# Kernel tuning notes

Hardware: AMD Instinct MI355X
Metric: run time of the kernel (lower is better)

Reference implementation:

```python
import jax, jax.numpy as jnp
import numpy as np

VOXEL_SCALE = 20.0   # cfg.SPARSE3D.VOXEL_SCALE (metric -> voxel pixels)
POOLER_SCALE = 0.25  # cfg.MODEL.ROI_BOX_HEAD.POOLER_SCALES_SPATIAL[0]
RES = 7              # pooler resolution per axis
EPS = 1e-5           # BatchNorm eps


def _roi_align_3d(feat, boxes_px, batch_idx, res):
    """3D ROIAlign, sampling_ratio=1 (one trilinear sample per bin).
    feat: [B, X, Y, Z, C] channels-last; boxes_px: [N,6] = (x1,y1,z1,x2,y2,z2)
    in feature-map coordinates. Returns [N, C, res, res, res]."""
    B, X, Y, Z, C = feat.shape
    N = boxes_px.shape[0]
    start, end = boxes_px[:, :3], boxes_px[:, 3:]
    size = jnp.maximum(end - start, 1.0)            # [N,3] legacy min roi size
    binsz = size / res
    off = jnp.arange(res, dtype=boxes_px.dtype) + 0.5
    px = start[:, 0:1] + off[None, :] * binsz[:, 0:1]   # [N,res]
    py = start[:, 1:2] + off[None, :] * binsz[:, 1:2]
    pz = start[:, 2:3] + off[None, :] * binsz[:, 2:3]
    P = res * res * res
    PX = jnp.broadcast_to(px[:, :, None, None], (N, res, res, res)).reshape(N, P)
    PY = jnp.broadcast_to(py[:, None, :, None], (N, res, res, res)).reshape(N, P)
    PZ = jnp.broadcast_to(pz[:, None, None, :], (N, res, res, res)).reshape(N, P)

    def corners(p, dim):
        p0 = jnp.floor(p)
        frac = p - p0
        i0 = jnp.clip(p0.astype(jnp.int32), 0, dim - 1)
        i1 = jnp.clip(p0.astype(jnp.int32) + 1, 0, dim - 1)
        return i0, i1, frac

    x0, x1, lx = corners(PX, X)
    y0, y1, ly = corners(PY, Y)
    z0, z1, lz = corners(PZ, Z)
    feat_flat = feat.reshape(B * X * Y * Z, C)
    base = batch_idx.astype(jnp.int32)[:, None]          # [N,1]
    acc = jnp.zeros((N, P, C), feat.dtype)
    for dx in (0, 1):  # 8 trilinear corners; fixed small loop
        xi, wx = (x0, 1.0 - lx) if dx == 0 else (x1, lx)
        for dy in (0, 1):
            yi, wy = (y0, 1.0 - ly) if dy == 0 else (y1, ly)
            for dz in (0, 1):
                zi, wz = (z0, 1.0 - lz) if dz == 0 else (z1, lz)
                lin = ((base * X + xi) * Y + yi) * Z + zi  # [N,P]
                acc = acc + (wx * wy * wz)[:, :, None] * feat_flat[lin]
    pooled = acc.reshape(N, res, res, res, C)  # 1 sample per bin -> no avg
    return pooled.transpose(0, 4, 1, 2, 3)     # [N, C, rx, ry, rz]


def setup_inputs():
    key = jax.random.key(0)
    ks = jax.random.split(key, 8)
    B, C, X, Y, Z = 2, 128, 80, 80, 20
    N, rep = 1024, 128 * RES              # rep = OUT_CHANNELS * pooler_z = 896
    in_size = C * RES * RES * RES         # 43904
    features = jax.random.normal(ks[0], (B, X, Y, Z, C), jnp.float32)
    ext = jnp.array([16.0, 16.0, 4.0], jnp.float32)  # metric extent = dim/(voxel_scale*pooler_scale)
    ctr = jax.random.uniform(ks[1], (N, 3), jnp.float32) * ext
    half = 0.25 + jax.random.uniform(ks[2], (N, 3), jnp.float32) * 1.75
    boxes = jnp.concatenate([ctr - half, ctr + half], axis=1)  # metric units
    batch_idx = jax.random.randint(ks[3], (N,), 0, B, jnp.int32)
    conv_w = jax.random.normal(ks[4], (rep, C, RES), jnp.float32) * 0.02
    conv_b = jnp.zeros((rep,), jnp.float32)
    gamma = jnp.ones((rep,), jnp.float32)
    beta = jnp.zeros((rep,), jnp.float32)
    fc6_w = jax.random.normal(ks[5], (in_size, rep), jnp.float32) * np.float32(1.0 / np.sqrt(in_size))
    fc6_b = jnp.zeros((rep,), jnp.float32)
    fc7_w = jax.random.normal(ks[6], (rep, rep), jnp.float32) * np.float32(1.0 / np.sqrt(rep))
    fc7_b = jnp.zeros((rep,), jnp.float32)
    return dict(features=features, boxes=boxes, conv_w=conv_w, conv_b=conv_b,
                gamma=gamma, beta=beta, fc6_w=fc6_w, fc6_b=fc6_b,
                fc7_w=fc7_w, fc7_b=fc7_b, batch_idx=batch_idx)


def reference(features, boxes, conv_w, conv_b, gamma, beta,
              fc6_w, fc6_b, fc7_w, fc7_b, batch_idx):
    # convert_metric_to_pixel (x voxel_scale) fused with pooler spatial scale
    boxes_px = boxes * (VOXEL_SCALE * POOLER_SCALE)
    pooled = _roi_align_3d(features, boxes_px, batch_idx, RES)  # [N,C,7,7,7]
    # conv3d kernel [1,1,Z]: contract channels and z -> [N, rep, 7, 7]
    y = jnp.einsum('ncxyz,rcz->nrxy', pooled, conv_w) + conv_b[None, :, None, None]
    # BatchNorm3d, training-mode batch statistics per channel
    mu = y.mean(axis=(0, 2, 3), keepdims=True)
    var = ((y - mu) ** 2).mean(axis=(0, 2, 3), keepdims=True)
    y = (y - mu) * jax.lax.rsqrt(var + EPS) * gamma[None, :, None, None] + beta[None, :, None, None]
    y = jax.nn.relu(y)
    x2 = y.reshape(y.shape[0], -1)                   # [N, rep*49] == [N, C*343]
    x3 = jax.nn.relu(x2 @ fc6_w + fc6_b)
    x4 = jax.nn.relu(x3 @ fc7_w + fc7_b)
    return x4
```

## Files before the change

kernel.cpp:

```cpp
#include <hip/hip_runtime.h>
#include <cstdint>

typedef unsigned short u16;
using bf16x8  = __attribute__((ext_vector_type(8))) __bf16;
using floatx4 = __attribute__((ext_vector_type(4))) float;

__device__ __forceinline__ u16 f2bf(float f) {
    uint32_t u = __builtin_bit_cast(uint32_t, f);
    u += 0x7fffu + ((u >> 16) & 1u);
    return (u16)(u >> 16);
}
__device__ __forceinline__ float bf2f(u16 h) {
    uint32_t u = ((uint32_t)h) << 16;
    return __builtin_bit_cast(float, u);
}

__device__ __forceinline__ void gload16(const u16* g, u16* l) {
    __builtin_amdgcn_global_load_lds(
        (const __attribute__((address_space(1))) unsigned int*)g,
        (__attribute__((address_space(3))) unsigned int*)l,
        16, 0, 0);
}

__global__ __launch_bounds__(256) void k_roialign(
    const float* __restrict__ feat, const float* __restrict__ boxes,
    const int* __restrict__ bidx, u16* __restrict__ A1)
{
    const int n = blockIdx.x;
    const int t = threadIdx.x;
    const float s = 5.0f;
    const float x1 = boxes[n*6+0]*s, y1 = boxes[n*6+1]*s, z1 = boxes[n*6+2]*s;
    const float x2 = boxes[n*6+3]*s, y2 = boxes[n*6+4]*s, z2 = boxes[n*6+5]*s;
    const float binx = fmaxf(x2-x1, 1.0f) * (1.0f/7.0f);
    const float biny = fmaxf(y2-y1, 1.0f) * (1.0f/7.0f);
    const float binz = fmaxf(z2-z1, 1.0f) * (1.0f/7.0f);
    const int b = bidx[n];
    const float* fb = feat + (size_t)b * 80 * 80 * 20 * 128;
    const int c4   = (t & 31) * 4;
    const int slot = t >> 5;

    for (int p = slot; p < 343; p += 8) {
        const int xq = p / 49;
        const int rem = p - xq * 49;
        const int yq = rem / 7;
        const int zq = rem - yq * 7;
        const float px = x1 + ((float)xq + 0.5f) * binx;
        const float py = y1 + ((float)yq + 0.5f) * biny;
        const float pz = z1 + ((float)zq + 0.5f) * binz;
        const float fx = floorf(px), fy = floorf(py), fz = floorf(pz);
        const float lx = px - fx, ly = py - fy, lz = pz - fz;
        const int xi0 = min(max((int)fx,     0), 79);
        const int xi1 = min(max((int)fx + 1, 0), 79);
        const int yi0 = min(max((int)fy,     0), 79);
        const int yi1 = min(max((int)fy + 1, 0), 79);
        const int zi0 = min(max((int)fz,     0), 19);
        const int zi1 = min(max((int)fz + 1, 0), 19);
        const float wx0 = 1.f-lx, wy0 = 1.f-ly, wz0 = 1.f-lz;
        const float w00 = wx0*wy0, w01 = wx0*ly, w10 = lx*wy0, w11 = lx*ly;
        float a0=0.f, a1=0.f, a2=0.f, a3=0.f;
#define RC(W, XI, YI, ZI) { \
        const float4 v = *(const float4*)(fb + (size_t)(((XI)*80+(YI))*20+(ZI))*128 + c4); \
        a0 = fmaf((W), v.x, a0); a1 = fmaf((W), v.y, a1); \
        a2 = fmaf((W), v.z, a2); a3 = fmaf((W), v.w, a3); }
        RC(w00*wz0, xi0, yi0, zi0); RC(w00*lz, xi0, yi0, zi1);
        RC(w01*wz0, xi0, yi1, zi0); RC(w01*lz, xi0, yi1, zi1);
        RC(w10*wz0, xi1, yi0, zi0); RC(w10*lz, xi1, yi0, zi1);
        RC(w11*wz0, xi1, yi1, zi0); RC(w11*lz, xi1, yi1, zi1);
#undef RC
        const int m = n * 49 + xq * 7 + yq;
        ushort4 o;
        o.x = f2bf(a0); o.y = f2bf(a1); o.z = f2bf(a2); o.w = f2bf(a3);
        *(ushort4*)(A1 + (size_t)m * 896 + zq * 128 + c4) = o;
    }
}

__global__ __launch_bounds__(256) void k_prep_wc(
    const float* __restrict__ w, u16* __restrict__ out)
{
    const int i = blockIdx.x * 256 + threadIdx.x;
    const int r = i / 896, k = i % 896;
    const int z = k >> 7, c = k & 127;
    out[i] = f2bf(w[(r * 128 + c) * 7 + z]);
}

template <int PERM>
__global__ __launch_bounds__(256) void k_transpose(
    const float* __restrict__ in, u16* __restrict__ out, int Kin)
{
    __shared__ u16 tile[64][72];
    const int kp0 = blockIdx.x * 64, r0 = blockIdx.y * 64;
    const int t = threadIdx.x;
#pragma unroll
    for (int it = 0; it < 16; ++it) {
        const int idx = it * 256 + t;
        const int i = idx >> 6, rl = idx & 63;
        const int kp = kp0 + i;
        const int k = PERM ? (kp % 896) * 49 + (kp / 896) : kp;
        tile[i][rl] = f2bf(in[(size_t)k * 896 + r0 + rl]);
    }
    __syncthreads();
#pragma unroll
    for (int it = 0; it < 16; ++it) {
        const int idx = it * 256 + t;
        const int rl = idx >> 6, i = idx & 63;
        out[(size_t)(r0 + rl) * Kin + kp0 + i] = tile[i][rl];
    }
}

template <int EPI>
__global__ __launch_bounds__(256) void k_gemm(
    const u16* __restrict__ A, const u16* __restrict__ Bt,
    float* __restrict__ outF, u16* __restrict__ outH,
    const float* __restrict__ bias, float* __restrict__ bnsum, float* __restrict__ bnsq,
    int Astride, int Bstride, int kpc, int ktot, int partStride)
{
    __shared__ __align__(16) u16 lA[128 * 32];
    __shared__ __align__(16) u16 lB[128 * 32];
    const int t = threadIdx.x;
    const int wave = t >> 6, lane = t & 63;
    const int wm = wave & 1, wn = wave >> 1;
    const int quad = lane >> 4, lr = lane & 15;

    int mt, nt, kz;
    if (EPI == 0) {
        const int wg = blockIdx.x;
        const int swz = (wg & 7) * 343 + (wg >> 3);
        nt = swz % 7; mt = swz / 7; kz = 0;
    } else {
        mt = blockIdx.x; nt = blockIdx.y; kz = blockIdx.z;
    }
    const size_t m0 = (size_t)mt * 128;
    const size_t n0 = (size_t)nt * 128;
    const int kbeg = kz * kpc;
    const int kend = min(kbeg + kpc, ktot);

    floatx4 acc[4][4];
    const floatx4 zero = {0.f, 0.f, 0.f, 0.f};
#pragma unroll
    for (int a = 0; a < 4; ++a)
#pragma unroll
        for (int bq = 0; bq < 4; ++bq) acc[a][bq] = zero;

    const int ch0 = wave * 2, ch1 = ch0 + 1;
    const int sr0 = ch0 * 16 + (lane >> 2);
    const int sr1 = sr0 + 16;
    const int sc  = (lane & 3) * 8;
    const u16* gA0 = A  + (m0 + sr0) * (size_t)Astride + (size_t)kbeg * 32 + sc;
    const u16* gA1 = A  + (m0 + sr1) * (size_t)Astride + (size_t)kbeg * 32 + sc;
    const u16* gB0 = Bt + (n0 + sr0) * (size_t)Bstride + (size_t)kbeg * 32 + sc;
    const u16* gB1 = Bt + (n0 + sr1) * (size_t)Bstride + (size_t)kbeg * 32 + sc;
    u16* lA0 = lA + ch0 * 512;
    u16* lA1 = lA + ch1 * 512;
    u16* lB0 = lB + ch0 * 512;
    u16* lB1 = lB + ch1 * 512;

    for (int ks = kbeg; ks < kend; ++ks) {
        __syncthreads();
        gload16(gA0, lA0); gload16(gA1, lA1);
        gload16(gB0, lB0); gload16(gB1, lB1);
        gA0 += 32; gA1 += 32; gB0 += 32; gB1 += 32;
        __syncthreads();
        bf16x8 af[4], bfr[4];
#pragma unroll
        for (int mt4 = 0; mt4 < 4; ++mt4)
            af[mt4] = *(const bf16x8*)(lA + (wm * 64 + mt4 * 16 + lr) * 32 + quad * 8);
#pragma unroll
        for (int nt4 = 0; nt4 < 4; ++nt4)
            bfr[nt4] = *(const bf16x8*)(lB + (wn * 64 + nt4 * 16 + lr) * 32 + quad * 8);
#pragma unroll
        for (int mt4 = 0; mt4 < 4; ++mt4)
#pragma unroll
            for (int nt4 = 0; nt4 < 4; ++nt4)
                acc[mt4][nt4] = __builtin_amdgcn_mfma_f32_16x16x32_bf16(
                    af[mt4], bfr[nt4], acc[mt4][nt4], 0, 0, 0);
    }

    if (EPI == 0) {
#pragma unroll
        for (int nt4 = 0; nt4 < 4; ++nt4) {
            const int n = (int)n0 + wn * 64 + nt4 * 16 + lr;
            const float bv = bias[n];
            float s1 = 0.f, s2 = 0.f;
#pragma unroll
            for (int mt4 = 0; mt4 < 4; ++mt4) {
#pragma unroll
                for (int j = 0; j < 4; ++j) {
                    const int m = (int)m0 + wm * 64 + mt4 * 16 + quad * 4 + j;
                    const float v = acc[mt4][nt4][j] + bv;
                    outH[(size_t)m * 896 + n] = f2bf(v);
                    s1 += v;
                    s2 = fmaf(v, v, s2);
                }
            }
            s1 += __shfl_xor(s1, 16); s1 += __shfl_xor(s1, 32);
            s2 += __shfl_xor(s2, 16); s2 += __shfl_xor(s2, 32);
            if (quad == 0) {
                atomicAdd(&bnsum[n], s1);
                atomicAdd(&bnsq[n],  s2);
            }
        }
    } else {
        float* po = outF + (size_t)blockIdx.z * partStride;
#pragma unroll
        for (int nt4 = 0; nt4 < 4; ++nt4) {
            const int n = (int)n0 + wn * 64 + nt4 * 16 + lr;
#pragma unroll
            for (int mt4 = 0; mt4 < 4; ++mt4) {
#pragma unroll
                for (int j = 0; j < 4; ++j) {
                    const int m = (int)m0 + wm * 64 + mt4 * 16 + quad * 4 + j;
                    po[(size_t)m * 896 + n] = acc[mt4][nt4][j];
                }
            }
        }
    }
}

__global__ __launch_bounds__(256) void k_bn_apply(
    u16* __restrict__ y, const float* __restrict__ s1, const float* __restrict__ s2,
    const float* __restrict__ gamma, const float* __restrict__ beta)
{
    const size_t i = ((size_t)blockIdx.x * 256 + threadIdx.x) * 8;
    uint4 d = *(const uint4*)(y + i);
    const u16* h = (const u16*)&d;
    const int r0 = (int)(i % 896);
    __align__(16) u16 o[8];
    const float invM = 1.0f / 50176.0f;
#pragma unroll
    for (int j = 0; j < 8; ++j) {
        const int r = r0 + j;
        const float mu  = s1[r] * invM;
        const float var = fmaf(-mu, mu, s2[r] * invM);
        const float rs  = rsqrtf(var + 1e-5f);
        const float v   = (bf2f(h[j]) - mu) * rs * gamma[r] + beta[r];
        o[j] = f2bf(fmaxf(v, 0.f));
    }
    *(uint4*)(y + i) = *(const uint4*)o;
}

__global__ __launch_bounds__(256) void k_x3(
    const float* __restrict__ part, const float* __restrict__ bias, u16* __restrict__ x3)
{
    const size_t i = ((size_t)blockIdx.x * 256 + threadIdx.x) * 4;
    float a0=0.f, a1=0.f, a2=0.f, a3=0.f;
#pragma unroll
    for (int c = 0; c < 16; ++c) {
        const float4 v = *(const float4*)(part + (size_t)c * 917504 + i);
        a0 += v.x; a1 += v.y; a2 += v.z; a3 += v.w;
    }
    const int r = (int)(i % 896);
    ushort4 o;
    o.x = f2bf(fmaxf(a0 + bias[r+0], 0.f));
    o.y = f2bf(fmaxf(a1 + bias[r+1], 0.f));
    o.z = f2bf(fmaxf(a2 + bias[r+2], 0.f));
    o.w = f2bf(fmaxf(a3 + bias[r+3], 0.f));
    *(ushort4*)(x3 + i) = o;
}

__global__ __launch_bounds__(256) void k_out(
    const float* __restrict__ part, const float* __restrict__ bias, float* __restrict__ out)
{
    const size_t i = ((size_t)blockIdx.x * 256 + threadIdx.x) * 4;
    float a0=0.f, a1=0.f, a2=0.f, a3=0.f;
#pragma unroll
    for (int c = 0; c < 4; ++c) {
        const float4 v = *(const float4*)(part + (size_t)c * 917504 + i);
        a0 += v.x; a1 += v.y; a2 += v.z; a3 += v.w;
    }
    const int r = (int)(i % 896);
    float4 o;
    o.x = fmaxf(a0 + bias[r+0], 0.f);
    o.y = fmaxf(a1 + bias[r+1], 0.f);
    o.z = fmaxf(a2 + bias[r+2], 0.f);
    o.w = fmaxf(a3 + bias[r+3], 0.f);
    *(float4*)(out + i) = o;
}

extern "C" void kernel_launch(void* const* d_in, const int* in_sizes, int n_in,
                              void* d_out, int out_size, void* d_ws, size_t ws_size,
                              hipStream_t stream)
{
    (void)in_sizes; (void)n_in; (void)out_size; (void)ws_size;
    const float* features = (const float*)d_in[0];
    const float* boxes    = (const float*)d_in[1];
    const float* conv_w   = (const float*)d_in[2];
    const float* conv_b   = (const float*)d_in[3];
    const float* gamma    = (const float*)d_in[4];
    const float* beta     = (const float*)d_in[5];
    const float* fc6_w    = (const float*)d_in[6];
    const float* fc6_b    = (const float*)d_in[7];
    const float* fc7_w    = (const float*)d_in[8];
    const float* fc7_b    = (const float*)d_in[9];
    const int*   batch_idx = (const int*)d_in[10];
    float* out = (float*)d_out;
    char* ws = (char*)d_ws;

    size_t off = 0;
    auto alloc = [&](size_t b) { size_t o = off; off += (b + 255) & ~(size_t)255; return o; };
    const size_t oA1   = alloc(50176ull * 896 * 2);
    const size_t oWcT  = alloc(896ull * 896 * 2);
    const size_t oY    = alloc(50176ull * 896 * 2);
    const size_t oF6T  = alloc(43904ull * 896 * 2);
    const size_t oF7T  = alloc(896ull * 896 * 2);
    const size_t oStat = alloc(8192);
    const size_t oP2 = oA1;
    const size_t oX3 = oA1 + 58720256;
    const size_t oP3 = oX3 + 1835008;

    u16*   A1    = (u16*)(ws + oA1);
    u16*   WcT   = (u16*)(ws + oWcT);
    u16*   Y     = (u16*)(ws + oY);
    u16*   F6T   = (u16*)(ws + oF6T);
    u16*   F7T   = (u16*)(ws + oF7T);
    float* bnsum = (float*)(ws + oStat);
    float* bnsq  = bnsum + 1024;
    float* P2    = (float*)(ws + oP2);
    u16*   X3    = (u16*)(ws + oX3);
    float* P3    = (float*)(ws + oP3);

    k_prep_wc<<<3136, 256, 0, stream>>>(conv_w, WcT);
    k_transpose<1><<<dim3(686, 14), 256, 0, stream>>>(fc6_w, F6T, 43904);
    k_transpose<0><<<dim3(14, 14), 256, 0, stream>>>(fc7_w, F7T, 896);
    hipMemsetAsync(ws + oStat, 0, 8192, stream);

    k_roialign<<<1024, 256, 0, stream>>>(features, boxes, batch_idx, A1);

    k_gemm<0><<<dim3(2744, 1, 1), 256, 0, stream>>>(
        A1, WcT, nullptr, Y, conv_b, bnsum, bnsq, 896, 896, 28, 28, 0);

    k_bn_apply<<<21952, 256, 0, stream>>>(Y, bnsum, bnsq, gamma, beta);

    k_gemm<1><<<dim3(8, 7, 16), 256, 0, stream>>>(
        Y, F6T, P2, nullptr, nullptr, nullptr, nullptr, 43904, 43904, 86, 1372, 917504);
    k_x3<<<896, 256, 0, stream>>>(P2, fc6_b, X3);

    k_gemm<1><<<dim3(8, 7, 4), 256, 0, stream>>>(
        X3, F7T, P3, nullptr, nullptr, nullptr, nullptr, 896, 896, 7, 28, 917504);
    k_out<<<896, 256, 0, stream>>>(P3, fc7_b, out);
}
```

Baseline: 770.1 us.

## Double-buffer GEMM LDS staging and raise split-K factors for FC layers

Doubles the LDS tiles in the shared GEMM kernel so the next K-slice is fetched with global_load_lds while MFMAs run on the current one, replacing two barriers per step with one wait plus barrier. It also raises the split-K count for fc6 from 16 to 24 and for fc7 from 4 to 7, giving more workgroups on the GPU, and moves the reduction kernels and workspace offsets to match. The cost is twice the LDS per block, which may lower occupancy, and more partial-sum traffic in the reduction kernels.

Result: no change. 760.5 us (-1.3%).

```diff
diff --git a/kernel.cpp b/kernel.cpp
--- a/kernel.cpp
+++ b/kernel.cpp
@@ -114,8 +114,8 @@
     const float* __restrict__ bias, float* __restrict__ bnsum, float* __restrict__ bnsq,
     int Astride, int Bstride, int kpc, int ktot, int partStride)
 {
-    __shared__ __align__(16) u16 lA[128 * 32];
-    __shared__ __align__(16) u16 lB[128 * 32];
+    __shared__ __align__(16) u16 lA[2 * 128 * 32];
+    __shared__ __align__(16) u16 lB[2 * 128 * 32];
     const int t = threadIdx.x;
     const int wave = t >> 6, lane = t & 63;
     const int wm = wave & 1, wn = wave >> 1;
@@ -149,31 +149,42 @@
     const u16* gA1 = A  + (m0 + sr1) * (size_t)Astride + (size_t)kbeg * 32 + sc;
     const u16* gB0 = Bt + (n0 + sr0) * (size_t)Bstride + (size_t)kbeg * 32 + sc;
     const u16* gB1 = Bt + (n0 + sr1) * (size_t)Bstride + (size_t)kbeg * 32 + sc;
-    u16* lA0 = lA + ch0 * 512;
-    u16* lA1 = lA + ch1 * 512;
-    u16* lB0 = lB + ch0 * 512;
-    u16* lB1 = lB + ch1 * 512;
-
+    const int lo0 = ch0 * 512, lo1 = ch1 * 512;
+
+#define STAGE(buf) { \
+    u16* la_ = lA + (buf) * 4096; u16* lb_ = lB + (buf) * 4096; \
+    gload16(gA0, la_ + lo0); gload16(gA1, la_ + lo1); \
+    gload16(gB0, lb_ + lo0); gload16(gB1, lb_ + lo1); \
+    gA0 += 32; gA1 += 32; gB0 += 32; gB1 += 32; }
+
+    STAGE(0);
+    asm volatile("s_waitcnt vmcnt(0)" ::: "memory");
+    __builtin_amdgcn_s_barrier();
+
+    int cur = 0;
     for (int ks = kbeg; ks < kend; ++ks) {
-        __syncthreads();
-        gload16(gA0, lA0); gload16(gA1, lA1);
-        gload16(gB0, lB0); gload16(gB1, lB1);
-        gA0 += 32; gA1 += 32; gB0 += 32; gB1 += 32;
-        __syncthreads();
+        if (ks + 1 < kend) STAGE(cur ^ 1);
+        asm volatile("" ::: "memory");
+        const u16* la = lA + cur * 4096;
+        const u16* lb = lB + cur * 4096;
         bf16x8 af[4], bfr[4];
 #pragma unroll
         for (int mt4 = 0; mt4 < 4; ++mt4)
-            af[mt4] = *(const bf16x8*)(lA + (wm * 64 + mt4 * 16 + lr) * 32 + quad * 8);
+            af[mt4] = *(const bf16x8*)(la + (wm * 64 + mt4 * 16 + lr) * 32 + quad * 8);
 #pragma unroll
         for (int nt4 = 0; nt4 < 4; ++nt4)
-            bfr[nt4] = *(const bf16x8*)(lB + (wn * 64 + nt4 * 16 + lr) * 32 + quad * 8);
+            bfr[nt4] = *(const bf16x8*)(lb + (wn * 64 + nt4 * 16 + lr) * 32 + quad * 8);
 #pragma unroll
         for (int mt4 = 0; mt4 < 4; ++mt4)
 #pragma unroll
             for (int nt4 = 0; nt4 < 4; ++nt4)
                 acc[mt4][nt4] = __builtin_amdgcn_mfma_f32_16x16x32_bf16(
                     af[mt4], bfr[nt4], acc[mt4][nt4], 0, 0, 0);
-    }
+        asm volatile("s_waitcnt vmcnt(0)" ::: "memory");
+        __builtin_amdgcn_s_barrier();
+        cur ^= 1;
+    }
+#undef STAGE
 
     if (EPI == 0) {
 #pragma unroll
@@ -244,7 +255,7 @@
     const size_t i = ((size_t)blockIdx.x * 256 + threadIdx.x) * 4;
     float a0=0.f, a1=0.f, a2=0.f, a3=0.f;
 #pragma unroll
-    for (int c = 0; c < 16; ++c) {
+    for (int c = 0; c < 24; ++c) {
         const float4 v = *(const float4*)(part + (size_t)c * 917504 + i);
         a0 += v.x; a1 += v.y; a2 += v.z; a3 += v.w;
     }
@@ -263,7 +274,7 @@
     const size_t i = ((size_t)blockIdx.x * 256 + threadIdx.x) * 4;
     float a0=0.f, a1=0.f, a2=0.f, a3=0.f;
 #pragma unroll
-    for (int c = 0; c < 4; ++c) {
+    for (int c = 0; c < 7; ++c) {
         const float4 v = *(const float4*)(part + (size_t)c * 917504 + i);
         a0 += v.x; a1 += v.y; a2 += v.z; a3 += v.w;
     }
@@ -304,8 +315,8 @@
     const size_t oF7T  = alloc(896ull * 896 * 2);
     const size_t oStat = alloc(8192);
     const size_t oP2 = oA1;
-    const size_t oX3 = oA1 + 58720256;
-    const size_t oP3 = oX3 + 1835008;
+    const size_t oX3 = oA1 + 88080384;
+    const size_t oP3 = oA1;
 
     u16*   A1    = (u16*)(ws + oA1);
     u16*   WcT   = (u16*)(ws + oWcT);
@@ -330,11 +341,11 @@
 
     k_bn_apply<<<21952, 256, 0, stream>>>(Y, bnsum, bnsq, gamma, beta);
 
-    k_gemm<1><<<dim3(8, 7, 16), 256, 0, stream>>>(
-        Y, F6T, P2, nullptr, nullptr, nullptr, nullptr, 43904, 43904, 86, 1372, 917504);
+    k_gemm<1><<<dim3(8, 7, 24), 256, 0, stream>>>(
+        Y, F6T, P2, nullptr, nullptr, nullptr, nullptr, 43904, 43904, 58, 1372, 917504);
     k_x3<<<896, 256, 0, stream>>>(P2, fc6_b, X3);
 
-    k_gemm<1><<<dim3(8, 7, 4), 256, 0, stream>>>(
-        X3, F7T, P3, nullptr, nullptr, nullptr, nullptr, 896, 896, 7, 28, 917504);
+    k_gemm<1><<<dim3(8, 7, 7), 256, 0, stream>>>(
+        X3, F7T, P3, nullptr, nullptr, nullptr, nullptr, 896, 896, 4, 28, 917504);
     k_out<<<896, 256, 0, stream>>>(P3, fc7_b, out);
 }
```
